# Kernel tuning notes

Measured on AMD Instinct MI355X. Metric: run time of the kernel, lower is better.

## Reference

```python
import jax, jax.numpy as jnp
import numpy as np

TEMPERATURE = 0.5
B, D = 4096, 256


def setup_inputs() -> dict:
    key = jax.random.key(0)
    k1, k2 = jax.random.split(key)
    z_i = jax.random.normal(k1, (B, D), dtype=jnp.float32)
    z_j = jax.random.normal(k2, (B, D), dtype=jnp.float32)
    return {"z_i": z_i, "z_j": z_j}


def reference(z_i, z_j):
    batch = z_i.shape[0]
    n = 2 * batch
    z = jnp.concatenate([z_i, z_j], axis=0)                      # [2B, D]
    z = z / jnp.linalg.norm(z, axis=1, keepdims=True)            # L2-normalize rows
    # cosine_similarity of unit vectors == dot product -> single GEMM
    sim = jnp.einsum('id,jd->ij', z, z) / TEMPERATURE            # [2B, 2B]
    mask = jnp.eye(n, dtype=bool)
    sim = jnp.where(mask, -jnp.inf, sim)                         # mask self-similarity
    positives = jnp.concatenate(
        [jnp.diagonal(sim, offset=batch), jnp.diagonal(sim, offset=-batch)], axis=0
    )                                                            # [2B]
    loss = -positives + jax.nn.logsumexp(sim, axis=1)            # [2B]
    return loss.mean()
```

## Files before the change

kernel.cpp:

```cpp
#include <hip/hip_runtime.h>
#include <hip/hip_bf16.h>
#include <stdint.h>
#include <stddef.h>


#define B_ROWS 4096
#define D_DIM  256
#define N_ROWS 8192
#define BM 128
#define BN 128

typedef __bf16 bf16;
typedef bf16  bf16x8  __attribute__((ext_vector_type(8)));
typedef bf16  bf16x4  __attribute__((ext_vector_type(4)));
typedef float floatx4 __attribute__((ext_vector_type(4)));

__global__ __launch_bounds__(256) void normalize_kernel(
    const float* __restrict__ z_i, const float* __restrict__ z_j,
    bf16* __restrict__ zn, float* __restrict__ sumexp) {
  const int wave = threadIdx.x >> 6;
  const int lane = threadIdx.x & 63;
  const int row  = blockIdx.x * 4 + wave;
  const float* src = (row < B_ROWS) ? (z_i + (size_t)row * D_DIM)
                                    : (z_j + (size_t)(row - B_ROWS) * D_DIM);
  float4 v = ((const float4*)src)[lane];
  float ss = v.x * v.x + v.y * v.y + v.z * v.z + v.w * v.w;
  #pragma unroll
  for (int m = 1; m < 64; m <<= 1) ss += __shfl_xor(ss, m);
  const float rn = rsqrtf(ss) * 1.6986436f;
  bf16x4 o;
  o[0] = (bf16)(v.x * rn);
  o[1] = (bf16)(v.y * rn);
  o[2] = (bf16)(v.z * rn);
  o[3] = (bf16)(v.w * rn);
  ((bf16x4*)(zn + (size_t)row * D_DIM))[lane] = o;
  if (lane == 0) sumexp[row] = 0.f;
}

__global__ __launch_bounds__(512, 2) void simexp_kernel(
    const bf16* __restrict__ zn, float* __restrict__ sumexp,
    float* __restrict__ pos) {
  __shared__ __align__(16) bf16 Bs[2][BN * D_DIM];

  const int tid   = threadIdx.x;
  const int wave  = tid >> 6;
  const int lane  = tid & 63;
  const int lcol  = lane & 15;
  const int lquad = lane >> 4;
  const int wr = (wave >> 1) * 32;
  const int wc = (wave & 1) * 64;
  const int ri = blockIdx.x >> 2;
  const int cj = blockIdx.x & 3;
  const int row_base = ri * BM;
  const bool has_tail = (ri < 32 && cj >= 2);

  auto ct_of = [&](int t) { return (ri + 8 * cj + t) & 63; };

  auto stageB = [&](int buf, const bf16* src, int it0, int it1) {
    for (int it = it0; it < it1; ++it) {
      const int s   = it * 512 + tid;
      const int n   = s >> 5;
      const int kcs = s & 31;
      const int kc  = (kcs & 24) | ((kcs & 7) ^ (n & 7));
      __builtin_amdgcn_global_load_lds(
          (const __attribute__((address_space(1))) unsigned int*)
              (src + (size_t)n * D_DIM + kc * 8),
          (__attribute__((address_space(3))) unsigned int*)&Bs[buf][s * 8],
          16, 0, 0);
    }
  };

  stageB(0, zn + (size_t)row_base * D_DIM, 0, 8);
  stageB(1, zn + (size_t)ct_of(0) * BM * D_DIM, 0, 8);
  __syncthreads();

  floatx4 af[2][8];
  #pragma unroll
  for (int ti = 0; ti < 2; ++ti) {
    const int n = wr + ti * 16 + lcol;
    #pragma unroll
    for (int kq = 0; kq < 8; ++kq) {
      const int kc  = kq * 4 + lquad;
      const int kcs = (kc & 24) | ((kc & 7) ^ (n & 7));
      af[ti][kq] = *(const floatx4*)(&Bs[0][(n * 32 + kcs) * 8]);
    }
  }
  __syncthreads();

  float rowsum[2][4];
  #pragma unroll
  for (int ti = 0; ti < 2; ++ti)
    #pragma unroll
    for (int r = 0; r < 4; ++r) rowsum[ti][r] = 0.f;

#define MFMA_(A, B_, C) __builtin_amdgcn_mfma_f32_16x16x32_bf16( \
    __builtin_bit_cast(bf16x8, A), B_, C, 0, 0, 0)

#define QPHASE(ACC, Q)                                                    \
  {                                                                       \
    bf16x8 bfr[8];                                                        \
    const int n = wc + (Q) * 16 + lcol;                                   \
    _Pragma("unroll")                                                     \
    for (int kq = 0; kq < 8; ++kq) {                                      \
      const int kc  = kq * 4 + lquad;                                     \
      const int kcs = (kc & 24) | ((kc & 7) ^ (n & 7));                   \
      bfr[kq] = *(const bf16x8*)(bbase + n * D_DIM + kcs * 8);            \
    }                                                                     \
    ACC[0] = floatx4{0.f, 0.f, 0.f, 0.f};                                 \
    ACC[1] = floatx4{0.f, 0.f, 0.f, 0.f};                                 \
    _Pragma("unroll")                                                     \
    for (int kq = 0; kq < 8; ++kq) {                                      \
      ACC[0] = MFMA_(af[0][kq], bfr[kq], ACC[0]);                         \
      ACC[1] = MFMA_(af[1][kq], bfr[kq], ACC[1]);                         \
    }                                                                     \
  }

#define SLICE(ACC, Q, CB, DG)                                             \
  {                                                                       \
    float cs = 0.f;                                                       \
    _Pragma("unroll")                                                     \
    for (int ti = 0; ti < 2; ++ti) {                                      \
      _Pragma("unroll")                                                   \
      for (int r = 0; r < 4; ++r) {                                       \
        const float v = ACC[ti][r];                                       \
        float e = __builtin_amdgcn_exp2f(v);                              \
        if (DG) {                                                         \
          const int rg = row_base + wr + ti * 16 + lquad * 4 + r;         \
          const int cg = (CB) + wc + (Q) * 16 + lcol;                     \
          if (cg == rg) e = 0.f;                \
        }                                                                 \
        rowsum[ti][r] += e;                                               \
        cs += e;                                                          \
      }                                                                   \
    }                                                                     \
    cs += __shfl_xor(cs, 16);                                             \
    cs += __shfl_xor(cs, 32);                                             \
    if (!(DG) && lquad == 0)                                              \
      atomicAdd(&sumexp[(CB) + wc + (Q) * 16 + lcol], cs);                \
  }

  floatx4 a3[2];
  int  pcol3  = 0;
  bool pdiag3 = false;

  #pragma unroll 1
  for (int t = 0; t < 8; ++t) {
    const bf16* bbase = &Bs[(t + 1) & 1][0];
    const int sb = t & 1;
    if (t < 7) {
      stageB(sb, zn + (size_t)ct_of(t + 1) * BM * D_DIM, 0, 8);
    } else if (has_tail) {
      stageB(sb, zn + (size_t)((ri + 32) * BM + (cj - 2) * 64) * D_DIM, 0, 4);
    }
    const int  colb = ct_of(t) * BM;
    const bool diag = (cj == 0 && t == 0);

    floatx4 a0[2], a1[2], a2[2];
    QPHASE(a0, 0)
    if (t > 0) SLICE(a3, 3, pcol3, pdiag3)
    QPHASE(a1, 1)
    SLICE(a0, 0, colb, diag)
    QPHASE(a2, 2)
    SLICE(a1, 1, colb, diag)
    QPHASE(a3, 3)
    SLICE(a2, 2, colb, diag)
    pcol3 = colb;
    pdiag3 = diag;
    __syncthreads();
  }
  SLICE(a3, 3, pcol3, pdiag3)

  if (has_tail && wc == 0) {
    const int colb = (ri + 32) * BM + (cj - 2) * 64;
    const bf16* bbase = &Bs[1][0];
    floatx4 ta[2];
    #pragma unroll
    for (int Q = 0; Q < 4; ++Q) {
      QPHASE(ta, Q)
      float cs = 0.f;
      #pragma unroll
      for (int ti = 0; ti < 2; ++ti) {
        #pragma unroll
        for (int r = 0; r < 4; ++r) {
          const float v = ta[ti][r];
          const float e = __builtin_amdgcn_exp2f(v);
          const int rg = row_base + wr + ti * 16 + lquad * 4 + r;
          const int cg = colb + Q * 16 + lcol;
          if (cg == rg + B_ROWS) {
            const float p = v * 0.6931471805599453f;
            pos[rg] = p;
            pos[cg] = p;
          }
          rowsum[ti][r] += e;
          cs += e;
        }
      }
      cs += __shfl_xor(cs, 16);
      cs += __shfl_xor(cs, 32);
      if (lquad == 0) atomicAdd(&sumexp[colb + Q * 16 + lcol], cs);
    }
  }
#undef SLICE
#undef QPHASE
#undef MFMA_

  #pragma unroll
  for (int ti = 0; ti < 2; ++ti) {
    #pragma unroll
    for (int r = 0; r < 4; ++r) {
      float s2 = rowsum[ti][r];
      s2 += __shfl_xor(s2, 1);
      s2 += __shfl_xor(s2, 2);
      s2 += __shfl_xor(s2, 4);
      s2 += __shfl_xor(s2, 8);
      if (lcol == 0) {
        const int grow = row_base + wr + ti * 16 + lquad * 4 + r;
        atomicAdd(&sumexp[grow], s2);
      }
    }
  }
}

__global__ __launch_bounds__(1024) void reduce_kernel(
    const float* __restrict__ sumexp, const float* __restrict__ pos,
    float* __restrict__ out) {
  __shared__ float ws[16];
  const int tid = threadIdx.x;
  float s = 0.f;
  const float ln2 = 0.6931471805599453f;
  for (int k = tid; k < N_ROWS; k += 1024)
    s += __builtin_amdgcn_logf(sumexp[k]) * ln2 - pos[k];
  #pragma unroll
  for (int m = 1; m < 64; m <<= 1) s += __shfl_xor(s, m);
  const int wave = tid >> 6, lane = tid & 63;
  if (lane == 0) ws[wave] = s;
  __syncthreads();
  if (wave == 0) {
    float t = (lane < 16) ? ws[lane] : 0.f;
    #pragma unroll
    for (int m = 1; m < 16; m <<= 1) t += __shfl_xor(t, m);
    if (lane == 0) out[0] = t * (1.0f / N_ROWS);
  }
}

extern "C" void kernel_launch(void* const* d_in, const int* in_sizes, int n_in,
                              void* d_out, int out_size, void* d_ws,
                              size_t ws_size, hipStream_t stream) {
  const float* z_i = (const float*)d_in[0];
  const float* z_j = (const float*)d_in[1];
  float* out = (float*)d_out;

  bf16* zn = (bf16*)d_ws;
  float* sumexp = (float*)((char*)d_ws + (size_t)N_ROWS * D_DIM * sizeof(bf16));
  float* pos = sumexp + N_ROWS;

  normalize_kernel<<<N_ROWS / 4, 256, 0, stream>>>(z_i, z_j, zn, sumexp);
  simexp_kernel<<<256, 512, 0, stream>>>(zn, sumexp, pos);
  reduce_kernel<<<1, 1024, 0, stream>>>(sumexp, pos, out);
}
```

Baseline: 92.08 us.

## Fuse final reduction into simexp kernel via last-block ticket; wait only on first stage

Removes the separate single-block reduce kernel launch. Each simexp block bumps a global ticket after fencing its atomics, and the last block reads sumexp/pos with atomic loads and computes the mean loss, reusing shared memory as scratch. The ticket is reset in the normalize kernel. The initial barrier now waits only for the first tile's loads (vmcnt(8)), so the second buffer's prefetch overlaps the A-fragment reads. This adds a serialized tail in one block plus extra fences.

```diff
diff --git a/kernel.cpp b/kernel.cpp
--- a/kernel.cpp
+++ b/kernel.cpp
@@ -17,10 +17,12 @@
 
 __global__ __launch_bounds__(256) void normalize_kernel(
     const float* __restrict__ z_i, const float* __restrict__ z_j,
-    bf16* __restrict__ zn, float* __restrict__ sumexp) {
+    bf16* __restrict__ zn, float* __restrict__ sumexp,
+    unsigned* __restrict__ ticket) {
   const int wave = threadIdx.x >> 6;
   const int lane = threadIdx.x & 63;
   const int row  = blockIdx.x * 4 + wave;
+  if (blockIdx.x == 0 && threadIdx.x == 0) *ticket = 0u;
   const float* src = (row < B_ROWS) ? (z_i + (size_t)row * D_DIM)
                                     : (z_j + (size_t)(row - B_ROWS) * D_DIM);
   float4 v = ((const float4*)src)[lane];
@@ -39,8 +41,10 @@
 
 __global__ __launch_bounds__(512, 2) void simexp_kernel(
     const bf16* __restrict__ zn, float* __restrict__ sumexp,
-    float* __restrict__ pos) {
+    float* __restrict__ pos, unsigned* __restrict__ ticket,
+    float* __restrict__ out) {
   __shared__ __align__(16) bf16 Bs[2][BN * D_DIM];
+  __shared__ unsigned s_last;
 
   const int tid   = threadIdx.x;
   const int wave  = tid >> 6;
@@ -72,7 +76,9 @@
 
   stageB(0, zn + (size_t)row_base * D_DIM, 0, 8);
   stageB(1, zn + (size_t)ct_of(0) * BM * D_DIM, 0, 8);
-  __syncthreads();
+  asm volatile("s_waitcnt vmcnt(8)" ::: "memory");
+  __builtin_amdgcn_sched_barrier(0);
+  __builtin_amdgcn_s_barrier();
 
   floatx4 af[2][8];
   #pragma unroll
@@ -219,27 +225,35 @@
       }
     }
   }
-}
-
-__global__ __launch_bounds__(1024) void reduce_kernel(
-    const float* __restrict__ sumexp, const float* __restrict__ pos,
-    float* __restrict__ out) {
-  __shared__ float ws[16];
-  const int tid = threadIdx.x;
-  float s = 0.f;
-  const float ln2 = 0.6931471805599453f;
-  for (int k = tid; k < N_ROWS; k += 1024)
-    s += __builtin_amdgcn_logf(sumexp[k]) * ln2 - pos[k];
-  #pragma unroll
-  for (int m = 1; m < 64; m <<= 1) s += __shfl_xor(s, m);
-  const int wave = tid >> 6, lane = tid & 63;
-  if (lane == 0) ws[wave] = s;
+
+  __threadfence();
   __syncthreads();
-  if (wave == 0) {
-    float t = (lane < 16) ? ws[lane] : 0.f;
-    #pragma unroll
-    for (int m = 1; m < 16; m <<= 1) t += __shfl_xor(t, m);
-    if (lane == 0) out[0] = t * (1.0f / N_ROWS);
+  if (tid == 0) s_last = (atomicAdd(ticket, 1u) == 255u) ? 1u : 0u;
+  __syncthreads();
+  if (s_last) {
+    __threadfence();
+    const float ln2 = 0.6931471805599453f;
+    float s = 0.f;
+    #pragma unroll
+    for (int it = 0; it < 16; ++it) {
+      const int k = it * 512 + tid;
+      const float se = __hip_atomic_load(&sumexp[k], __ATOMIC_RELAXED,
+                                         __HIP_MEMORY_SCOPE_AGENT);
+      const float pp = __hip_atomic_load(&pos[k], __ATOMIC_RELAXED,
+                                         __HIP_MEMORY_SCOPE_AGENT);
+      s += __builtin_amdgcn_logf(se) * ln2 - pp;
+    }
+    #pragma unroll
+    for (int m = 1; m < 64; m <<= 1) s += __shfl_xor(s, m);
+    float* ws = (float*)&Bs[0][0];
+    if (lane == 0) ws[wave] = s;
+    __syncthreads();
+    if (wave == 0) {
+      float tt = (lane < 8) ? ws[lane] : 0.f;
+      #pragma unroll
+      for (int m = 1; m < 8; m <<= 1) tt += __shfl_xor(tt, m);
+      if (lane == 0) out[0] = tt * (1.0f / N_ROWS);
+    }
   }
 }
 
@@ -253,8 +267,9 @@
   bf16* zn = (bf16*)d_ws;
   float* sumexp = (float*)((char*)d_ws + (size_t)N_ROWS * D_DIM * sizeof(bf16));
   float* pos = sumexp + N_ROWS;
-
-  normalize_kernel<<<N_ROWS / 4, 256, 0, stream>>>(z_i, z_j, zn, sumexp);
-  simexp_kernel<<<256, 512, 0, stream>>>(zn, sumexp, pos);
-  reduce_kernel<<<1, 1024, 0, stream>>>(sumexp, pos, out);
+  unsigned* ticket = (unsigned*)(pos + N_ROWS);
+
+  normalize_kernel<<<N_ROWS / 4, 256, 0, stream>>>(z_i, z_j, zn, sumexp,
+                                                   ticket);
+  simexp_kernel<<<256, 512, 0, stream>>>(zn, sumexp, pos, ticket, out);
 }
```

Measured after the change: 121.2 us. 31.6% more time.
